# Optimization experiments

Hardware: AMD Instinct MI355X
Metric: run time of the kernel (lower is better)

Reference implementation:

```python
import jax, jax.numpy as jnp
import numpy as np

B, S, H = 8, 4096, 1024
N_IDX = 65536
N_SEG = 8192


def setup_inputs() -> dict:
    key = jax.random.key(0)
    k1, k2, k3, k4, k5 = jax.random.split(key, 5)
    transformer_hidden = jax.random.normal(k1, (B, S, H), dtype=jnp.float32)
    indices = jax.random.randint(k2, (N_IDX,), 0, B * S, dtype=jnp.int32)
    segment_ids = jnp.sort(jax.random.randint(k3, (N_IDX,), 0, N_SEG, dtype=jnp.int32))
    W_dense = jax.random.normal(k4, (H, H), dtype=jnp.float32) * (1.0 / np.sqrt(H))
    b_dense = jnp.zeros((H,), dtype=jnp.float32)
    W_proj = jax.random.normal(k5, (1, H), dtype=jnp.float32) * (1.0 / np.sqrt(H))
    b_proj = jnp.zeros((1,), dtype=jnp.float32)
    return {
        "transformer_hidden": transformer_hidden,
        "indices": indices,
        "segment_ids": segment_ids,
        "W_dense": W_dense,
        "b_dense": b_dense,
        "W_proj": W_proj,
        "b_proj": b_proj,
    }


def reference(transformer_hidden, indices, segment_ids, W_dense, b_dense, W_proj, b_proj):
    # Flatten tokens: [B*S, H]
    hid = transformer_hidden.reshape(-1, transformer_hidden.shape[-1])
    # Ragged gather of grouped token indices, then per-group mean (segment mean)
    gathered = hid[indices]  # [n_idx, H]
    sums = jax.ops.segment_sum(gathered, segment_ids, num_segments=N_SEG)  # [G, H]
    counts = jax.ops.segment_sum(
        jnp.ones((indices.shape[0],), dtype=hid.dtype), segment_ids, num_segments=N_SEG
    )
    h = sums / jnp.maximum(counts, 1.0)[:, None]  # [G, H] group means
    # dense -> gelu (torch exact erf gelu) -> lin_proj -> flatten
    z = jax.nn.gelu(h @ W_dense.T + b_dense, approximate=False)
    predictions = z @ W_proj.T + b_proj  # [G, 1]
    return predictions.reshape(-1)
```

## Files before the change

### kernel.cpp

```cpp
#include <hip/hip_runtime.h>
#include <stdint.h>

#define BH   (8 * 4096)
#define HDIM 1024
#define NIDX 65536
#define NSEG 8192
#define KD   1024
#define ND   1024

typedef __bf16 bf16x8 __attribute__((ext_vector_type(8)));
typedef float  f32x4  __attribute__((ext_vector_type(4)));

__device__ __forceinline__ unsigned short f2bf(float f) {
  unsigned int u = __float_as_uint(f);
  u += 0x7fffu + ((u >> 16) & 1u);
  return (unsigned short)(u >> 16);
}

__device__ __forceinline__ void async16(const void* g, void* l) {
  __builtin_amdgcn_global_load_lds(
      (const __attribute__((address_space(1))) void*)g,
      (__attribute__((address_space(3))) void*)l,
      16, 0, 0);
}

__global__ void prep_kernel(const float* __restrict__ W, unsigned short* __restrict__ Wb,
                            const int* __restrict__ seg, int* __restrict__ starts) {
  if (blockIdx.x < 1024) {
    int i = (blockIdx.x * 256 + threadIdx.x) * 4;
    float4 v = *(const float4*)(W + i);
    ushort4 o;
    o.x = f2bf(v.x); o.y = f2bf(v.y); o.z = f2bf(v.z); o.w = f2bf(v.w);
    *(ushort4*)(Wb + i) = o;
  } else {
    int i = (blockIdx.x - 1024) * 256 + threadIdx.x;
    if (i > NIDX) return;
    int prev = (i == 0) ? -1 : seg[i - 1];
    int cur  = (i == NIDX) ? NSEG : seg[i];
    for (int g = prev + 1; g <= cur; ++g) starts[g] = i;
  }
}

__global__ void segmean_kernel(const float* __restrict__ hid,
                               const int* __restrict__ indices,
                               const int* __restrict__ starts,
                               unsigned short* __restrict__ hb,
                               float* __restrict__ out,
                               const float* __restrict__ b_proj) {
  const int g = blockIdx.x;
  const int t = threadIdx.x;
  const int start = starts[g];
  const int end   = starts[g + 1];
  const int col   = t * 4;

  float4 a0 = make_float4(0.f, 0.f, 0.f, 0.f);
  float4 a1 = a0, a2 = a0, a3 = a0;

  int i = start;
  for (; i + 4 <= end; i += 4) {
    int r0 = indices[i];
    int r1 = indices[i + 1];
    int r2 = indices[i + 2];
    int r3 = indices[i + 3];
    float4 v0 = *(const float4*)(hid + (size_t)r0 * HDIM + col);
    float4 v1 = *(const float4*)(hid + (size_t)r1 * HDIM + col);
    float4 v2 = *(const float4*)(hid + (size_t)r2 * HDIM + col);
    float4 v3 = *(const float4*)(hid + (size_t)r3 * HDIM + col);
    a0.x += v0.x; a0.y += v0.y; a0.z += v0.z; a0.w += v0.w;
    a1.x += v1.x; a1.y += v1.y; a1.z += v1.z; a1.w += v1.w;
    a2.x += v2.x; a2.y += v2.y; a2.z += v2.z; a2.w += v2.w;
    a3.x += v3.x; a3.y += v3.y; a3.z += v3.z; a3.w += v3.w;
  }
  for (; i < end; ++i) {
    int r = indices[i];
    float4 v = *(const float4*)(hid + (size_t)r * HDIM + col);
    a0.x += v.x; a0.y += v.y; a0.z += v.z; a0.w += v.w;
  }
  a0.x += a1.x + a2.x + a3.x;
  a0.y += a1.y + a2.y + a3.y;
  a0.z += a1.z + a2.z + a3.z;
  a0.w += a1.w + a2.w + a3.w;

  const float inv = 1.0f / fmaxf((float)(end - start), 1.0f);
  ushort4 o;
  o.x = f2bf(a0.x * inv); o.y = f2bf(a0.y * inv);
  o.z = f2bf(a0.z * inv); o.w = f2bf(a0.w * inv);
  *(ushort4*)(hb + (size_t)g * HDIM + col) = o;

  if (t == 0) out[g] = b_proj[0];
}

__global__ void __launch_bounds__(512)
gemm_gelu_proj_kernel(const unsigned short* __restrict__ A,
                      const unsigned short* __restrict__ Bw,
                      const float* __restrict__ b_dense,
                      const float* __restrict__ w_proj,
                      float* __restrict__ out) {
  __shared__ alignas(16) unsigned short As[128 * 128];
  __shared__ alignas(16) unsigned short Bs[128 * 128];

  const int tid  = threadIdx.x;
  const int lane = tid & 63;
  const int wave = tid >> 6;
  const int wm   = wave >> 2;
  const int wn   = wave & 3;
  const int m0   = blockIdx.x * 128;
  const int n0   = blockIdx.y * 128;
  const int lr   = lane & 15;
  const int quad = lane >> 4;

  f32x4 acc[4][2];
#pragma unroll
  for (int mi = 0; mi < 4; ++mi)
#pragma unroll
    for (int ni = 0; ni < 2; ++ni) {
      acc[mi][ni][0] = 0.f; acc[mi][ni][1] = 0.f;
      acc[mi][ni][2] = 0.f; acc[mi][ni][3] = 0.f;
    }

  for (int kt = 0; kt < KD / 128; ++kt) {
    const int k0 = kt * 128;
#pragma unroll
    for (int j = 0; j < 4; ++j) {
      int c   = j * 512 + wave * 64 + lane;
      int row = c >> 4, sl = c & 15;
      int kcg = sl ^ (row & 15);
      async16(A + (size_t)(m0 + row) * KD + k0 + kcg * 8,
              (char*)As + (j * 512 + wave * 64) * 16);
    }
#pragma unroll
    for (int j = 0; j < 4; ++j) {
      int c   = j * 512 + wave * 64 + lane;
      int row = c >> 4, sl = c & 15;
      int kcg = sl ^ (row & 15);
      async16(Bw + (size_t)(n0 + row) * KD + k0 + kcg * 8,
              (char*)Bs + (j * 512 + wave * 64) * 16);
    }
    __syncthreads();

#pragma unroll
    for (int s = 0; s < 4; ++s) {
      bf16x8 af[4], bf_[2];
#pragma unroll
      for (int i = 0; i < 4; ++i) {
        int ra   = wm * 64 + i * 16 + lr;
        int slot = (s * 4 + quad) ^ (ra & 15);
        af[i] = *(const bf16x8*)(As + ra * 128 + slot * 8);
      }
#pragma unroll
      for (int i = 0; i < 2; ++i) {
        int rb   = wn * 32 + i * 16 + lr;
        int slot = (s * 4 + quad) ^ (rb & 15);
        bf_[i] = *(const bf16x8*)(Bs + rb * 128 + slot * 8);
      }
#pragma unroll
      for (int mi = 0; mi < 4; ++mi)
#pragma unroll
        for (int ni = 0; ni < 2; ++ni)
          acc[mi][ni] = __builtin_amdgcn_mfma_f32_16x16x32_bf16(af[mi], bf_[ni], acc[mi][ni], 0, 0, 0);
    }
    __syncthreads();
  }

#pragma unroll
  for (int mi = 0; mi < 4; ++mi) {
    float rp[4] = {0.f, 0.f, 0.f, 0.f};
#pragma unroll
    for (int ni = 0; ni < 2; ++ni) {
      int col  = n0 + wn * 32 + ni * 16 + lr;
      float bd = b_dense[col];
      float wp = w_proj[col];
#pragma unroll
      for (int r = 0; r < 4; ++r) {
        float v  = acc[mi][ni][r] + bd;
        float gl = 0.5f * v * (1.0f + erff(v * 0.70710678118654752f));
        rp[r] += gl * wp;
      }
    }
#pragma unroll
    for (int r = 0; r < 4; ++r) {
      float c = rp[r];
      c += __shfl_xor(c, 1);
      c += __shfl_xor(c, 2);
      c += __shfl_xor(c, 4);
      c += __shfl_xor(c, 8);
      if (lr == 0)
        atomicAdd(out + (m0 + wm * 64 + mi * 16 + quad * 4 + r), c);
    }
  }
}

extern "C" void kernel_launch(void* const* d_in, const int* in_sizes, int n_in,
                              void* d_out, int out_size, void* d_ws, size_t ws_size,
                              hipStream_t stream) {
  const float* hid     = (const float*)d_in[0];
  const int*   indices = (const int*)d_in[1];
  const int*   seg     = (const int*)d_in[2];
  const float* W_dense = (const float*)d_in[3];
  const float* b_dense = (const float*)d_in[4];
  const float* W_proj  = (const float*)d_in[5];
  const float* b_proj  = (const float*)d_in[6];
  float* out = (float*)d_out;

  unsigned short* hb     = (unsigned short*)d_ws;
  unsigned short* Wb     = (unsigned short*)((char*)d_ws + (size_t)NSEG * KD * 2);
  int*            starts = (int*)((char*)d_ws + (size_t)NSEG * KD * 2 + (size_t)ND * KD * 2);

  prep_kernel<<<dim3(1024 + (NIDX + 256) / 256), 256, 0, stream>>>(W_dense, Wb, seg, starts);
  segmean_kernel<<<dim3(NSEG), 256, 0, stream>>>(hid, indices, starts, hb, out, b_proj);
  gemm_gelu_proj_kernel<<<dim3(NSEG / 128, ND / 128), 512, 0, stream>>>(hb, Wb, b_dense, W_proj, out);
}
```

Measured before the change: 233.8 us.

## Pre-convert hidden states to bf16 before the gather and prefetch indices

The prep kernel now converts the whole fp32 hidden tensor to bf16 in workspace. The segment-mean kernel then gathers half-width bf16 rows and widens them to fp32 for accumulation. The gather loop also software-pipelines the index loads one iteration ahead. The aim is to halve gather traffic, but it adds a full streaming pass over the hidden tensor (fp32 read plus bf16 write) and extra rounding before the mean, and it needs much more workspace.

```diff
diff --git a/kernel.cpp b/kernel.cpp
--- a/kernel.cpp
+++ b/kernel.cpp
@@ -17,6 +17,10 @@
   return (unsigned short)(u >> 16);
 }
 
+__device__ __forceinline__ float bf2f(unsigned short u) {
+  return __uint_as_float((unsigned int)u << 16);
+}
+
 __device__ __forceinline__ void async16(const void* g, void* l) {
   __builtin_amdgcn_global_load_lds(
       (const __attribute__((address_space(1))) void*)g,
@@ -24,16 +28,24 @@
       16, 0, 0);
 }
 
-__global__ void prep_kernel(const float* __restrict__ W, unsigned short* __restrict__ Wb,
+__global__ void prep_kernel(const float* __restrict__ hid, unsigned short* __restrict__ hidb,
+                            const float* __restrict__ W, unsigned short* __restrict__ Wb,
                             const int* __restrict__ seg, int* __restrict__ starts) {
-  if (blockIdx.x < 1024) {
-    int i = (blockIdx.x * 256 + threadIdx.x) * 4;
+  const int b = blockIdx.x;
+  if (b < 32768) {
+    int i = (b * 256 + threadIdx.x) * 4;
+    float4 v = *(const float4*)(hid + (size_t)i);
+    ushort4 o;
+    o.x = f2bf(v.x); o.y = f2bf(v.y); o.z = f2bf(v.z); o.w = f2bf(v.w);
+    *(ushort4*)(hidb + (size_t)i) = o;
+  } else if (b < 32768 + 1024) {
+    int i = ((b - 32768) * 256 + threadIdx.x) * 4;
     float4 v = *(const float4*)(W + i);
     ushort4 o;
     o.x = f2bf(v.x); o.y = f2bf(v.y); o.z = f2bf(v.z); o.w = f2bf(v.w);
     *(ushort4*)(Wb + i) = o;
   } else {
-    int i = (blockIdx.x - 1024) * 256 + threadIdx.x;
+    int i = (b - 32768 - 1024) * 256 + threadIdx.x;
     if (i > NIDX) return;
     int prev = (i == 0) ? -1 : seg[i - 1];
     int cur  = (i == NIDX) ? NSEG : seg[i];
@@ -41,7 +53,7 @@
   }
 }
 
-__global__ void segmean_kernel(const float* __restrict__ hid,
+__global__ void segmean_kernel(const unsigned short* __restrict__ hidb,
                                const int* __restrict__ indices,
                                const int* __restrict__ starts,
                                unsigned short* __restrict__ hb,
@@ -57,24 +69,27 @@
   float4 a1 = a0, a2 = a0, a3 = a0;
 
   int i = start;
-  for (; i + 4 <= end; i += 4) {
-    int r0 = indices[i];
-    int r1 = indices[i + 1];
-    int r2 = indices[i + 2];
-    int r3 = indices[i + 3];
-    float4 v0 = *(const float4*)(hid + (size_t)r0 * HDIM + col);
-    float4 v1 = *(const float4*)(hid + (size_t)r1 * HDIM + col);
-    float4 v2 = *(const float4*)(hid + (size_t)r2 * HDIM + col);
-    float4 v3 = *(const float4*)(hid + (size_t)r3 * HDIM + col);
-    a0.x += v0.x; a0.y += v0.y; a0.z += v0.z; a0.w += v0.w;
-    a1.x += v1.x; a1.y += v1.y; a1.z += v1.z; a1.w += v1.w;
-    a2.x += v2.x; a2.y += v2.y; a2.z += v2.z; a2.w += v2.w;
-    a3.x += v3.x; a3.y += v3.y; a3.z += v3.z; a3.w += v3.w;
+  int j0 = 0, j1 = 0, j2 = 0, j3 = 0;
+  bool have = (i + 4 <= end);
+  if (have) { j0 = indices[i]; j1 = indices[i + 1]; j2 = indices[i + 2]; j3 = indices[i + 3]; }
+  while (have) {
+    const int r0 = j0, r1 = j1, r2 = j2, r3 = j3;
+    i += 4;
+    have = (i + 4 <= end);
+    if (have) { j0 = indices[i]; j1 = indices[i + 1]; j2 = indices[i + 2]; j3 = indices[i + 3]; }
+    ushort4 u0 = *(const ushort4*)(hidb + (size_t)r0 * HDIM + col);
+    ushort4 u1 = *(const ushort4*)(hidb + (size_t)r1 * HDIM + col);
+    ushort4 u2 = *(const ushort4*)(hidb + (size_t)r2 * HDIM + col);
+    ushort4 u3 = *(const ushort4*)(hidb + (size_t)r3 * HDIM + col);
+    a0.x += bf2f(u0.x); a0.y += bf2f(u0.y); a0.z += bf2f(u0.z); a0.w += bf2f(u0.w);
+    a1.x += bf2f(u1.x); a1.y += bf2f(u1.y); a1.z += bf2f(u1.z); a1.w += bf2f(u1.w);
+    a2.x += bf2f(u2.x); a2.y += bf2f(u2.y); a2.z += bf2f(u2.z); a2.w += bf2f(u2.w);
+    a3.x += bf2f(u3.x); a3.y += bf2f(u3.y); a3.z += bf2f(u3.z); a3.w += bf2f(u3.w);
   }
   for (; i < end; ++i) {
-    int r = indices[i];
-    float4 v = *(const float4*)(hid + (size_t)r * HDIM + col);
-    a0.x += v.x; a0.y += v.y; a0.z += v.z; a0.w += v.w;
+    const int r = indices[i];
+    ushort4 u = *(const ushort4*)(hidb + (size_t)r * HDIM + col);
+    a0.x += bf2f(u.x); a0.y += bf2f(u.y); a0.z += bf2f(u.z); a0.w += bf2f(u.w);
   }
   a0.x += a1.x + a2.x + a3.x;
   a0.y += a1.y + a2.y + a3.y;
@@ -205,8 +220,12 @@
   unsigned short* hb     = (unsigned short*)d_ws;
   unsigned short* Wb     = (unsigned short*)((char*)d_ws + (size_t)NSEG * KD * 2);
   int*            starts = (int*)((char*)d_ws + (size_t)NSEG * KD * 2 + (size_t)ND * KD * 2);
-
-  prep_kernel<<<dim3(1024 + (NIDX + 256) / 256), 256, 0, stream>>>(W_dense, Wb, seg, starts);
-  segmean_kernel<<<dim3(NSEG), 256, 0, stream>>>(hid, indices, starts, hb, out, b_proj);
+  size_t off = (size_t)NSEG * KD * 2 + (size_t)ND * KD * 2 + (size_t)(NSEG + 1) * 4;
+  off = (off + 255) & ~(size_t)255;
+  unsigned short* hidb = (unsigned short*)((char*)d_ws + off);
+
+  prep_kernel<<<dim3(32768 + 1024 + (NIDX + 256) / 256), 256, 0, stream>>>(
+      hid, hidb, W_dense, Wb, seg, starts);
+  segmean_kernel<<<dim3(NSEG), 256, 0, stream>>>(hidb, indices, starts, hb, out, b_proj);
   gemm_gelu_proj_kernel<<<dim3(NSEG / 128, ND / 128), 512, 0, stream>>>(hb, Wb, b_dense, W_proj, out);
 }
```

New measurement: 251.1 us. 7.4% more time.
